# Kernel optimization log

Measured on AMD Instinct MI355X. Metric: run time of the kernel, lower is better.

Reference implementation:

```python
import jax, jax.numpy as jnp
import numpy as np

Q_AA = 21    # amino acids + gap
D_REP = 64   # representation dim
H = 32       # heads
L = 256      # sequence length
DK = 32
DV = 32
M = 8192     # number of MSA sequences
LAMBDA = 1e-3


def setup_inputs() -> dict:
    key = jax.random.key(0)
    ks = jax.random.split(key, 6)
    return {
        "reps_matrix": jax.random.normal(ks[0], (Q_AA, D_REP), jnp.float32),
        "Q": jax.random.normal(ks[1], (H, L, DK), jnp.float32),
        "K": jax.random.normal(ks[2], (H, L, DK), jnp.float32),
        "V_metric": jax.random.normal(ks[3], (H, D_REP, DV), jnp.float32),
        "Z": jax.random.randint(ks[4], (L, M), 0, Q_AA),
        "weights": jax.random.uniform(ks[5], (M,), jnp.float32),
    }


def reference(reps_matrix, Q, K, V_metric, Z, weights):
    dk = Q.shape[-1]
    # symmetrized per-head attention map (no mask)
    scores = jnp.einsum('hid,hjd->hij', Q, K) / jnp.sqrt(jnp.asarray(dk, Q.dtype))
    probs = jax.nn.softmax(scores, axis=-1)
    A = 0.5 * (probs + jnp.swapaxes(probs, -1, -2))        # (H, L, L)

    # V_aa via RBF kernel on V1 = reps_matrix @ V_metric
    V1 = jnp.einsum('qd,hdv->hqv', reps_matrix, V_metric)  # (H, q, dv)
    gamma = 1.0 / V1.shape[1]  # torch code uses 1/X.shape[1] == 1/q
    sq = jnp.sum(V1 * V1, axis=-1)                          # (H, q)
    D2 = sq[:, :, None] + sq[:, None, :] - 2.0 * jnp.einsum('hqv,hav->hqa', V1, V1)
    Vaa = jnp.exp(-gamma * jnp.maximum(D2, 0.0))           # (H, q, q)

    # coupling tensor J with zeroed diagonal (i == j)
    J = jnp.einsum('hij,hqa->ijqa', A, Vaa)                # (L, L, q, q)
    off_diag = 1.0 - jnp.eye(J.shape[0], dtype=J.dtype)
    J = J * off_diag[:, :, None, None]

    q = Vaa.shape[1]
    Zoh = jax.nn.one_hot(Z, q, dtype=J.dtype)              # (L, M, q)
    # energy[state, position, sequence] = sum_{j,a} J[r,j,state,a] * onehot(Z)[j,m,a]
    E = jnp.einsum('rjqa,jma->qrm', J, Zoh)                # (q, L, M)
    lge = jax.nn.logsumexp(E, axis=0)                      # (L, M)
    E_correct = jnp.take_along_axis(E, Z[None], axis=0)[0] # (L, M)

    pl = -jnp.sum(weights * jnp.sum(E_correct - lge, axis=0))
    reg = LAMBDA * jnp.sum(J * J)
    return pl + reg
```

## Files before the change

### kernel.cpp

```cpp
#include <hip/hip_runtime.h>
#include <hip/hip_bf16.h>

typedef unsigned int uint;
typedef float v2f __attribute__((ext_vector_type(2)));

#define H_ 32
#define L_ 256
#define DK_ 32
#define DV_ 32
#define QAA 21
#define AQ_ 441
#define DREP 64
#define M_ 8192
#define LAMBDA_ 1e-3f

#define JSTR 52
#define JJSTR 1104
#define JCH 8
#define CHUNK_B (JCH * JJSTR)
#define NGRAN (CHUNK_B / 16)
#define NCH (L_ / JCH)

#define JC 8
#define TM 4

__global__ __launch_bounds__(256) void softmax_kernel(const float* __restrict__ Q,
                                                      const float* __restrict__ K,
                                                      float* __restrict__ P) {
  const int i = blockIdx.x, h = blockIdx.y, j = threadIdx.x;
  __shared__ float qrow[DK_];
  __shared__ float red[256];
  if (j < DK_) qrow[j] = Q[(h * L_ + i) * DK_ + j];
  __syncthreads();
  const float* krow = &K[(h * L_ + j) * DK_];
  float s = 0.f;
#pragma unroll
  for (int d = 0; d < DK_; ++d) s += qrow[d] * krow[d];
  s *= 0.17677669529663687f;
  red[j] = s;
  __syncthreads();
  for (int t = 128; t > 0; t >>= 1) {
    if (j < t) red[j] = fmaxf(red[j], red[j + t]);
    __syncthreads();
  }
  const float mx = red[0];
  __syncthreads();
  const float e = __expf(s - mx);
  red[j] = e;
  __syncthreads();
  for (int t = 128; t > 0; t >>= 1) {
    if (j < t) red[j] += red[j + t];
    __syncthreads();
  }
  P[(h * L_ + i) * L_ + j] = e / red[0];
}

__global__ __launch_bounds__(256) void sym_kernel(const float* __restrict__ P,
                                                  float* __restrict__ A) {
  __shared__ float t1[32][33], t2[32][33];
  const int h = blockIdx.z;
  const int i0 = blockIdx.x * 32, j0 = blockIdx.y * 32;
  const int tx = threadIdx.x, ty = threadIdx.y;
#pragma unroll
  for (int ry = 0; ry < 4; ++ry) {
    const int row = ty + ry * 8;
    t1[row][tx] = P[(h * L_ + i0 + row) * L_ + j0 + tx];
    t2[row][tx] = P[(h * L_ + j0 + row) * L_ + i0 + tx];
  }
  __syncthreads();
#pragma unroll
  for (int ry = 0; ry < 4; ++ry) {
    const int row = ty + ry * 8;
    A[(h * L_ + i0 + row) * L_ + j0 + tx] = 0.5f * (t1[row][tx] + t2[tx][row]);
  }
}

__global__ __launch_bounds__(256) void vaa_kernel(const float* __restrict__ reps,
                                                  const float* __restrict__ Vm,
                                                  float* __restrict__ Vaa) {
  const int h = blockIdx.x;
  __shared__ float V1[QAA * DV_];
  __shared__ float sq[QAA];
  for (int e = threadIdx.x; e < QAA * DV_; e += 256) {
    const int q = e >> 5, v = e & 31;
    float acc = 0.f;
#pragma unroll
    for (int d = 0; d < DREP; ++d) acc += reps[q * DREP + d] * Vm[(h * DREP + d) * DV_ + v];
    V1[e] = acc;
  }
  __syncthreads();
  if (threadIdx.x < QAA) {
    float acc = 0.f;
#pragma unroll
    for (int v = 0; v < DV_; ++v) { const float x = V1[threadIdx.x * DV_ + v]; acc += x * x; }
    sq[threadIdx.x] = acc;
  }
  __syncthreads();
  const float gamma = 1.f / 21.f;
  for (int e = threadIdx.x; e < AQ_; e += 256) {
    const int qq = e / QAA, aa = e - qq * QAA;
    float dot = 0.f;
#pragma unroll
    for (int v = 0; v < DV_; ++v) dot += V1[qq * DV_ + v] * V1[aa * DV_ + v];
    const float d2 = sq[qq] + sq[aa] - 2.f * dot;
    Vaa[h * AQ_ + e] = __expf(-gamma * fmaxf(d2, 0.f));
  }
}

__global__ __launch_bounds__(256) void reg_kernel(const float* __restrict__ A,
                                                  const float* __restrict__ Vaa,
                                                  float* __restrict__ out) {
  const int h1 = blockIdx.x >> 5, h2 = blockIdx.x & 31;
  const float* A1 = A + h1 * (L_ * L_);
  const float* A2 = A + h2 * (L_ * L_);
  float s = 0.f;
  for (int idx = threadIdx.x; idx < L_ * L_; idx += 256) s += A1[idx] * A2[idx];
  s -= A1[threadIdx.x * (L_ + 1)] * A2[threadIdx.x * (L_ + 1)];
  float g = 0.f;
  const float* V1 = Vaa + h1 * AQ_;
  const float* V2 = Vaa + h2 * AQ_;
  for (int e = threadIdx.x; e < AQ_; e += 256) g += V1[e] * V2[e];
  __shared__ float redS[256], redG[256];
  redS[threadIdx.x] = s; redG[threadIdx.x] = g;
  __syncthreads();
  for (int t = 128; t > 0; t >>= 1) {
    if (threadIdx.x < t) {
      redS[threadIdx.x] += redS[threadIdx.x + t];
      redG[threadIdx.x] += redG[threadIdx.x + t];
    }
    __syncthreads();
  }
  if (threadIdx.x == 0) atomicAdd(out, LAMBDA_ * redS[0] * redG[0]);
}

static __device__ inline unsigned bf16_bits(float x) {
  __hip_bfloat16 b = __float2bfloat16(x);
  unsigned short u;
  __builtin_memcpy(&u, &b, 2);
  return (unsigned)u;
}

__global__ __launch_bounds__(256) void jbuild_kernel(const float* __restrict__ A,
                                                     const float* __restrict__ Vaa,
                                                     unsigned char* __restrict__ Jg) {
  __shared__ float AT[L_ * H_];
  const int r = blockIdx.x, tid = threadIdx.x;
#pragma unroll
  for (int i = 0; i < H_; ++i) AT[tid * H_ + i] = A[(i * L_ + r) * L_ + tid];

  const int s = tid;
  const bool active = (s < 231);
  int a = 0, w = 0;
  if (active) { a = s / 11; w = s - a * 11; }
  const int q0 = 2 * w, q1 = q0 + 1;
  float vh0[H_], vh1[H_];
#pragma unroll
  for (int h = 0; h < H_; ++h) {
    vh0[h] = (active && q0 < QAA) ? Vaa[h * AQ_ + a * QAA + q0] : 0.f;
    vh1[h] = (active && q1 < QAA) ? Vaa[h * AQ_ + a * QAA + q1] : 0.f;
  }
  __syncthreads();

  unsigned char* dst = Jg + (size_t)r * (L_ * JJSTR);
  const int byte_off = a * JSTR + w * 4;
  for (int j = 0; j < L_; ++j) {
    float v0 = 0.f, v1 = 0.f;
    const float4* Ar4 = (const float4*)&AT[j * H_];
#pragma unroll
    for (int h4 = 0; h4 < H_ / 4; ++h4) {
      const float4 a4 = Ar4[h4];
      v0 += a4.x * vh0[h4 * 4 + 0]; v1 += a4.x * vh1[h4 * 4 + 0];
      v0 += a4.y * vh0[h4 * 4 + 1]; v1 += a4.y * vh1[h4 * 4 + 1];
      v0 += a4.z * vh0[h4 * 4 + 2]; v1 += a4.z * vh1[h4 * 4 + 2];
      v0 += a4.w * vh0[h4 * 4 + 3]; v1 += a4.w * vh1[h4 * 4 + 3];
    }
    if (j == r) { v0 = 0.f; v1 = 0.f; }
    if (active) {
      const unsigned u = bf16_bits(v0) | (bf16_bits(v1) << 16);
      *(unsigned*)(dst + (size_t)(j * JJSTR + byte_off)) = u;
    }
  }
}

#define GLOAD16(ldst, gsrc)                                                            \
  __builtin_amdgcn_global_load_lds((const __attribute__((address_space(1))) void*)(gsrc), \
                                   (__attribute__((address_space(3))) void*)(ldst), 16, 0, 0)

__global__ __launch_bounds__(256, 3) void gather_kernel(const unsigned char* __restrict__ Jg,
                                                        const int* __restrict__ Z,
                                                        const float* __restrict__ W,
                                                        float* __restrict__ out) {
  __shared__ __align__(16) unsigned char buf[2][CHUNK_B];
  __shared__ float red[256];
  const int r = blockIdx.x, tid = threadIdx.x;
  const int mb = blockIdx.y * 1024 + tid * 4;
  const unsigned char* Jr = Jg + (size_t)r * (L_ * JJSTR);

  v2f E2[TM][11];
#pragma unroll
  for (int k = 0; k < TM; ++k)
#pragma unroll
    for (int w = 0; w < 11; ++w) E2[k][w] = (v2f){0.f, 0.f};

  {
    const unsigned char* src = Jr;
    GLOAD16(&buf[0][tid * 16], src + tid * 16);
    GLOAD16(&buf[0][(tid + 256) * 16], src + (tid + 256) * 16);
    if (tid < NGRAN - 512) GLOAD16(&buf[0][(tid + 512) * 16], src + (tid + 512) * 16);
  }

  for (int c = 0; c < NCH; ++c) {
    __syncthreads();
    if (c + 1 < NCH) {
      const unsigned char* src = Jr + (size_t)(c + 1) * CHUNK_B;
      unsigned char* db = buf[(c + 1) & 1];
      GLOAD16(db + tid * 16, src + tid * 16);
      GLOAD16(db + (tid + 256) * 16, src + (tid + 256) * 16);
      if (tid < NGRAN - 512) GLOAD16(db + (tid + 512) * 16, src + (tid + 512) * 16);
    }
    const unsigned char* pb = buf[c & 1];
    for (int jj = 0; jj < JCH; ++jj) {
      const int j = c * JCH + jj;
      const int4 za = *(const int4*)(Z + j * M_ + mb);
      const int aa[TM] = {za.x, za.y, za.z, za.w};
#pragma unroll
      for (int k = 0; k < TM; ++k) {
        const uint* row = (const uint*)(pb + jj * JJSTR + aa[k] * JSTR);
        uint u[11];
#pragma unroll
        for (int w = 0; w < 11; ++w) u[w] = row[w];
#pragma unroll
        for (int w = 0; w < 11; ++w) {
          v2f t;
          t.x = __uint_as_float(u[w] << 16);
          t.y = __uint_as_float(u[w] & 0xFFFF0000u);
          E2[k][w] += t;
        }
      }
    }
  }

  const int4 zr = *(const int4*)(Z + r * M_ + mb);
  const int zra[TM] = {zr.x, zr.y, zr.z, zr.w};
  const float4 w4 = *(const float4*)(W + mb);
  const float wa[TM] = {w4.x, w4.y, w4.z, w4.w};
  float contrib = 0.f;
#pragma unroll
  for (int k = 0; k < TM; ++k) {
    float ev[QAA];
#pragma unroll
    for (int w = 0; w < 10; ++w) { ev[2 * w] = E2[k][w].x; ev[2 * w + 1] = E2[k][w].y; }
    ev[20] = E2[k][10].x;
    float mx = ev[0];
#pragma unroll
    for (int q = 1; q < QAA; ++q) mx = fmaxf(mx, ev[q]);
    float s = 0.f;
#pragma unroll
    for (int q = 0; q < QAA; ++q) s += __expf(ev[q] - mx);
    const float lge = mx + __logf(s);
    float Ec = ev[0];
#pragma unroll
    for (int q = 1; q < QAA; ++q) Ec = (zra[k] == q) ? ev[q] : Ec;
    contrib += wa[k] * (Ec - lge);
  }
  red[tid] = contrib;
  __syncthreads();
  for (int t = 128; t > 0; t >>= 1) {
    if (tid < t) red[tid] += red[tid + t];
    __syncthreads();
  }
  if (tid == 0) atomicAdd(out, -red[0]);
}

__global__ __launch_bounds__(256) void main_kernel(const float* __restrict__ A,
                                                   const float* __restrict__ Vaa,
                                                   const int* __restrict__ Z,
                                                   const float* __restrict__ W,
                                                   float* __restrict__ out) {
  __shared__ float A_r[H_ * L_];
  __shared__ float J_s[JC * AQ_];
  __shared__ float red[256];

  const int r = blockIdx.x;
  const int tid = threadIdx.x;
  const int mbase = blockIdx.y * (TM * 256) + tid;

  for (int e = tid; e < H_ * L_; e += 256) {
    const int h = e >> 8, j = e & 255;
    A_r[e] = A[(h * L_ + r) * L_ + j];
  }
  const int aq0 = tid, aq1 = tid + 256;
  const bool has1 = (aq1 < AQ_);
  float vh0[H_], vh1[H_];
#pragma unroll
  for (int h = 0; h < H_; ++h) {
    vh0[h] = Vaa[h * AQ_ + aq0];
    vh1[h] = has1 ? Vaa[h * AQ_ + aq1] : 0.f;
  }
  __syncthreads();

  float E[TM][QAA];
#pragma unroll
  for (int k = 0; k < TM; ++k)
#pragma unroll
    for (int q = 0; q < QAA; ++q) E[k][q] = 0.f;

  for (int j0 = 0; j0 < L_; j0 += JC) {
#pragma unroll
    for (int jj = 0; jj < JC; ++jj) {
      const int j = j0 + jj;
      float v0 = 0.f, v1 = 0.f;
#pragma unroll
      for (int h = 0; h < H_; ++h) {
        const float a = A_r[h * L_ + j];
        v0 += a * vh0[h];
        v1 += a * vh1[h];
      }
      if (j == r) { v0 = 0.f; v1 = 0.f; }
      J_s[jj * AQ_ + aq0] = v0;
      if (has1) J_s[jj * AQ_ + aq1] = v1;
    }
    __syncthreads();
#pragma unroll
    for (int jj = 0; jj < JC; ++jj) {
      const int j = j0 + jj;
      int a[TM];
#pragma unroll
      for (int k = 0; k < TM; ++k) a[k] = Z[j * M_ + mbase + k * 256];
#pragma unroll
      for (int k = 0; k < TM; ++k) {
        const float* row = &J_s[jj * AQ_ + a[k] * QAA];
#pragma unroll
        for (int q = 0; q < QAA; ++q) E[k][q] += row[q];
      }
    }
    __syncthreads();
  }

  float contrib = 0.f;
#pragma unroll
  for (int k = 0; k < TM; ++k) {
    const int m = mbase + k * 256;
    float mx = -1e30f;
#pragma unroll
    for (int q = 0; q < QAA; ++q) mx = fmaxf(mx, E[k][q]);
    float s = 0.f;
#pragma unroll
    for (int q = 0; q < QAA; ++q) s += __expf(E[k][q] - mx);
    const float lge = mx + __logf(s);
    const int zr = Z[r * M_ + m];
    float Ec = 0.f;
#pragma unroll
    for (int q = 0; q < QAA; ++q) Ec = (q == zr) ? E[k][q] : Ec;
    contrib += W[m] * (Ec - lge);
  }
  red[tid] = contrib;
  __syncthreads();
  for (int t = 128; t > 0; t >>= 1) {
    if (tid < t) red[tid] += red[tid + t];
    __syncthreads();
  }
  if (tid == 0) atomicAdd(out, -red[0]);
}

extern "C" void kernel_launch(void* const* d_in, const int* in_sizes, int n_in,
                              void* d_out, int out_size, void* d_ws, size_t ws_size,
                              hipStream_t stream) {
  const float* reps = (const float*)d_in[0];
  const float* Q    = (const float*)d_in[1];
  const float* K    = (const float*)d_in[2];
  const float* Vm   = (const float*)d_in[3];
  const int*   Z    = (const int*)d_in[4];
  const float* W    = (const float*)d_in[5];
  float* out = (float*)d_out;

  float* P   = (float*)d_ws;
  float* A   = P + H_ * L_ * L_;
  float* Vaa = A + H_ * L_ * L_;
  (void)in_sizes; (void)n_in; (void)out_size;

  const size_t base = (size_t)2 * H_ * L_ * L_ * 4 + (size_t)H_ * AQ_ * 4;
  const size_t jg_off = (base + 255) & ~(size_t)255;
  const size_t need = jg_off + (size_t)L_ * L_ * JJSTR;

  hipMemsetAsync(out, 0, sizeof(float), stream);
  softmax_kernel<<<dim3(L_, H_), 256, 0, stream>>>(Q, K, P);
  sym_kernel<<<dim3(8, 8, H_), dim3(32, 8), 0, stream>>>(P, A);
  vaa_kernel<<<H_, 256, 0, stream>>>(reps, Vm, Vaa);
  reg_kernel<<<H_ * H_, 256, 0, stream>>>(A, Vaa, out);

  if (ws_size >= need) {
    unsigned char* Jg = (unsigned char*)d_ws + jg_off;
    jbuild_kernel<<<L_, 256, 0, stream>>>(A, Vaa, Jg);
    gather_kernel<<<dim3(L_, M_ / 1024), 256, 0, stream>>>(Jg, Z, W, out);
  } else {
    main_kernel<<<dim3(L_, M_ / (TM * 256)), 256, 0, stream>>>(A, Vaa, Z, W, out);
  }
}
```

Baseline: 871.7 us.

## Compact bf16 J in global, expand to fp32 in LDS via register-staged prefetch

The J table in global memory is repacked with a tighter stride (44 bytes per row instead of 52), which shrinks the bytes the gather kernel streams. Instead of async global-to-LDS copies, each thread loads the chunk into registers, converts bf16 to fp32 once, and writes fp32 rows into LDS two chunks ahead. The inner accumulation loop then reads fp32 pairs directly with no per-use unpacking, and occupancy hint rises to 4 blocks. In exchange, LDS per block doubles, and register staging costs more VGPRs and extra LDS write traffic.

```diff
diff --git a/kernel.cpp b/kernel.cpp
--- a/kernel.cpp
+++ b/kernel.cpp
@@ -14,11 +14,14 @@
 #define M_ 8192
 #define LAMBDA_ 1e-3f
 
-#define JSTR 52
-#define JJSTR 1104
+#define GROW 44
+#define GJ_BLK 928
+#define LROW 88
+#define LJ_BLK 1856
 #define JCH 8
-#define CHUNK_B (JCH * JJSTR)
-#define NGRAN (CHUNK_B / 16)
+#define GCH (JCH * GJ_BLK)
+#define NGRAN (GCH / 16)
+#define LCH (JCH * LJ_BLK)
 #define NCH (L_ / JCH)
 
 #define JC 8
@@ -139,6 +142,8 @@
   __builtin_memcpy(&u, &b, 2);
   return (unsigned)u;
 }
+static __device__ inline float lo16f(uint u) { return __uint_as_float(u << 16); }
+static __device__ inline float hi16f(uint u) { return __uint_as_float(u & 0xFFFF0000u); }
 
 __global__ __launch_bounds__(256) void jbuild_kernel(const float* __restrict__ A,
                                                      const float* __restrict__ Vaa,
@@ -161,8 +166,8 @@
   }
   __syncthreads();
 
-  unsigned char* dst = Jg + (size_t)r * (L_ * JJSTR);
-  const int byte_off = a * JSTR + w * 4;
+  unsigned char* dst = Jg + (size_t)r * (L_ * GJ_BLK);
+  const int byte_off = a * GROW + w * 4;
   for (int j = 0; j < L_; ++j) {
     float v0 = 0.f, v1 = 0.f;
     const float4* Ar4 = (const float4*)&AT[j * H_];
@@ -177,24 +182,20 @@
     if (j == r) { v0 = 0.f; v1 = 0.f; }
     if (active) {
       const unsigned u = bf16_bits(v0) | (bf16_bits(v1) << 16);
-      *(unsigned*)(dst + (size_t)(j * JJSTR + byte_off)) = u;
-    }
-  }
-}
-
-#define GLOAD16(ldst, gsrc)                                                            \
-  __builtin_amdgcn_global_load_lds((const __attribute__((address_space(1))) void*)(gsrc), \
-                                   (__attribute__((address_space(3))) void*)(ldst), 16, 0, 0)
-
-__global__ __launch_bounds__(256, 3) void gather_kernel(const unsigned char* __restrict__ Jg,
+      *(unsigned*)(dst + (size_t)(j * GJ_BLK + byte_off)) = u;
+    }
+  }
+}
+
+__global__ __launch_bounds__(256, 4) void gather_kernel(const unsigned char* __restrict__ Jg,
                                                         const int* __restrict__ Z,
                                                         const float* __restrict__ W,
                                                         float* __restrict__ out) {
-  __shared__ __align__(16) unsigned char buf[2][CHUNK_B];
+  __shared__ __align__(16) unsigned char lbuf[2][LCH];
   __shared__ float red[256];
   const int r = blockIdx.x, tid = threadIdx.x;
   const int mb = blockIdx.y * 1024 + tid * 4;
-  const unsigned char* Jr = Jg + (size_t)r * (L_ * JJSTR);
+  const unsigned char* Jr = Jg + (size_t)r * (L_ * GJ_BLK);
 
   v2f E2[TM][11];
 #pragma unroll
@@ -202,43 +203,56 @@
 #pragma unroll
     for (int w = 0; w < 11; ++w) E2[k][w] = (v2f){0.f, 0.f};
 
-  {
-    const unsigned char* src = Jr;
-    GLOAD16(&buf[0][tid * 16], src + tid * 16);
-    GLOAD16(&buf[0][(tid + 256) * 16], src + (tid + 256) * 16);
-    if (tid < NGRAN - 512) GLOAD16(&buf[0][(tid + 512) * 16], src + (tid + 512) * 16);
-  }
+  const bool has2 = (tid < NGRAN - 256);
+  uint4 sw0, sw1;
+
+#define LOADCH(c)                                        \
+  do {                                                   \
+    const uint4* src = (const uint4*)(Jr + (size_t)(c) * GCH); \
+    sw0 = src[tid];                                      \
+    if (has2) sw1 = src[tid + 256];                      \
+  } while (0)
+
+#define WRITECH(buf_)                                                     \
+  do {                                                                    \
+    unsigned char* db = (buf_);                                           \
+    float4 fa, fb;                                                        \
+    fa.x = lo16f(sw0.x); fa.y = hi16f(sw0.x); fa.z = lo16f(sw0.y); fa.w = hi16f(sw0.y); \
+    fb.x = lo16f(sw0.z); fb.y = hi16f(sw0.z); fb.z = lo16f(sw0.w); fb.w = hi16f(sw0.w); \
+    *(float4*)(db + tid * 32) = fa;                                       \
+    *(float4*)(db + tid * 32 + 16) = fb;                                  \
+    if (has2) {                                                           \
+      fa.x = lo16f(sw1.x); fa.y = hi16f(sw1.x); fa.z = lo16f(sw1.y); fa.w = hi16f(sw1.y); \
+      fb.x = lo16f(sw1.z); fb.y = hi16f(sw1.z); fb.z = lo16f(sw1.w); fb.w = hi16f(sw1.w); \
+      *(float4*)(db + (tid + 256) * 32) = fa;                             \
+      *(float4*)(db + (tid + 256) * 32 + 16) = fb;                        \
+    }                                                                     \
+  } while (0)
+
+  LOADCH(0);
+  WRITECH(lbuf[0]);
+  LOADCH(1);
+  __syncthreads();
 
   for (int c = 0; c < NCH; ++c) {
-    __syncthreads();
-    if (c + 1 < NCH) {
-      const unsigned char* src = Jr + (size_t)(c + 1) * CHUNK_B;
-      unsigned char* db = buf[(c + 1) & 1];
-      GLOAD16(db + tid * 16, src + tid * 16);
-      GLOAD16(db + (tid + 256) * 16, src + (tid + 256) * 16);
-      if (tid < NGRAN - 512) GLOAD16(db + (tid + 512) * 16, src + (tid + 512) * 16);
-    }
-    const unsigned char* pb = buf[c & 1];
+    if (c + 1 < NCH) WRITECH(lbuf[(c + 1) & 1]);
+    if (c + 2 < NCH) LOADCH(c + 2);
+    const unsigned char* pb = lbuf[c & 1];
     for (int jj = 0; jj < JCH; ++jj) {
       const int j = c * JCH + jj;
       const int4 za = *(const int4*)(Z + j * M_ + mb);
       const int aa[TM] = {za.x, za.y, za.z, za.w};
 #pragma unroll
       for (int k = 0; k < TM; ++k) {
-        const uint* row = (const uint*)(pb + jj * JJSTR + aa[k] * JSTR);
-        uint u[11];
-#pragma unroll
-        for (int w = 0; w < 11; ++w) u[w] = row[w];
-#pragma unroll
-        for (int w = 0; w < 11; ++w) {
-          v2f t;
-          t.x = __uint_as_float(u[w] << 16);
-          t.y = __uint_as_float(u[w] & 0xFFFF0000u);
-          E2[k][w] += t;
-        }
+        const v2f* row = (const v2f*)(pb + jj * LJ_BLK + aa[k] * LROW);
+#pragma unroll
+        for (int w = 0; w < 11; ++w) E2[k][w] += row[w];
       }
     }
-  }
+    __syncthreads();
+  }
+#undef LOADCH
+#undef WRITECH
 
   const int4 zr = *(const int4*)(Z + r * M_ + mb);
   const int zra[TM] = {zr.x, zr.y, zr.z, zr.w};
@@ -381,7 +395,7 @@
 
   const size_t base = (size_t)2 * H_ * L_ * L_ * 4 + (size_t)H_ * AQ_ * 4;
   const size_t jg_off = (base + 255) & ~(size_t)255;
-  const size_t need = jg_off + (size_t)L_ * L_ * JJSTR;
+  const size_t need = jg_off + (size_t)L_ * L_ * GJ_BLK;
 
   hipMemsetAsync(out, 0, sizeof(float), stream);
   softmax_kernel<<<dim3(L_, H_), 256, 0, stream>>>(Q, K, P);
```

Result: slower. 1.327 ms (+52.2%).
